# Kernel tuning notes

Measured on AMD Instinct MI355X. Metric: run time of the kernel, lower is better.

Reference implementation:

```python
import jax, jax.numpy as jnp
import numpy as np

N_FR, N_FV, N_REL, N_VAL, N_KN = 512, 512, 256, 256, 512
TOPK_FR, TOPK_FV, TOPK_REL, TOPK_VAL = 8, 8, 4, 6
EPS = 1e-8


def setup_inputs() -> dict:
    key = jax.random.key(0)
    k1, k2, k3, k4 = jax.random.split(key, 4)
    B, S, D, DS = 8, 2048, 2048, 64
    N = N_FR + N_FV + N_REL + N_VAL + N_KN  # 2304
    return {
        "x": jax.random.normal(k1, (B, S, D), dtype=jnp.float32),
        "importance": jax.random.uniform(k2, (B, S), dtype=jnp.float32),
        "W": jax.random.normal(k3, (DS, D), dtype=jnp.float32) * (1.0 / np.sqrt(D)),
        "b": jnp.zeros((DS,), dtype=jnp.float32),
        "neuron_emb": jax.random.normal(k4, (N, DS), dtype=jnp.float32) * 0.02,
    }


def _topk_sparsify(w, k):
    # w: [B, n] -> keep top-k values, zero the rest, renormalize to sum 1
    vals, idx = jax.lax.top_k(w, k)
    B = w.shape[0]
    sparse = jnp.zeros_like(w).at[jnp.arange(B)[:, None], idx].set(vals)
    return sparse / (sparse.sum(axis=-1, keepdims=True) + EPS)


def reference(x, importance, W, b, neuron_emb):
    # Projection (nn.Linear): [B,S,d_space]; dropout is identity in eval mode
    h = jnp.einsum('bsd,kd->bsk', x, W) + b
    # Normalized neuron embeddings (F.normalize along dim=-1)
    emb = neuron_emb / jnp.linalg.norm(neuron_emb, axis=-1, keepdims=True)
    # All routing logits in one shot: [B, S, total_neurons]
    all_logits = jnp.einsum('bsk,nk->bsn', h, emb)

    fr_end = N_FR
    fv_end = N_FR + N_FV
    rel_end = fv_end + N_REL
    val_end = rel_end + N_VAL

    fr_pref = jax.nn.softmax(all_logits[..., :fr_end], axis=-1)
    fv_pref = jax.nn.softmax(all_logits[..., fr_end:fv_end], axis=-1)
    rel_pref = jax.nn.softmax(all_logits[..., fv_end:rel_end], axis=-1)  # shared by Q and K
    val_pref = jax.nn.softmax(all_logits[..., rel_end:val_end], axis=-1)

    def dense(pref):
        return jnp.einsum('bs,bsn->bn', importance, pref)

    fr_w = _topk_sparsify(dense(fr_pref), TOPK_FR)
    fv_w = _topk_sparsify(dense(fv_pref), TOPK_FV)
    rel_d = dense(rel_pref)
    rq_w = _topk_sparsify(rel_d, TOPK_REL)
    rk_w = rq_w  # relational_Q and relational_K slices are identical
    val_w = _topk_sparsify(dense(val_pref), TOPK_VAL)

    # Concatenate the five per-batch routing weight vectors: [B, 512+512+256+256+256]
    return jnp.concatenate([fr_w, fv_w, rq_w, rk_w, val_w], axis=-1)
```

## Files before the change

### kernel.cpp

```cpp
#include <hip/hip_runtime.h>
#include <hip/hip_bf16.h>

#define B_    8
#define S_    2048
#define D_    2048
#define DS_   64
#define NUSED 1536
#define TOK   16384

typedef __attribute__((ext_vector_type(8))) short bf16x8;
typedef __attribute__((ext_vector_type(4))) float f32x4;

static constexpr int WS_ETF  = 0;
static constexpr int WS_HT   = 98304;
static constexpr int WS_PART = 2195456;
static constexpr int WS_PART2= 3768320;
static constexpr int WS_WF   = 3866624;

typedef __attribute__((address_space(1))) const void g_void;
typedef __attribute__((address_space(3))) void l_void;

__device__ inline short bf_hi(float f, float& rhi) {
    __hip_bfloat16 h = __float2bfloat16(f);
    rhi = __bfloat162float(h);
    return __builtin_bit_cast(short, h);
}
__device__ inline short bf_of(float f) {
    __hip_bfloat16 h = __float2bfloat16(f);
    return __builtin_bit_cast(short, h);
}
__device__ inline int sliceOfTile(int tile) {
    return tile < 32 ? 0 : tile < 64 ? 1 : tile < 80 ? 2 : 3;
}

__launch_bounds__(256)
__global__ void k_pre(const float* __restrict__ emb, const float* __restrict__ W,
                      short* __restrict__ etfrag, short* __restrict__ wfrag) {
    __shared__ float red[2][16][8];
    __shared__ float rn[2][16];
    const int tid = threadIdx.x;
    if (blockIdx.x < 48) {
        const int tl = tid >> 7, tid2 = tid & 127;
        const int kh = tid2 >> 6, lane = tid2 & 63;
        const int tile = blockIdx.x * 2 + tl;
        const int nl = lane & 15;
        const int n = tile * 16 + nl;
        const int kb = kh * 32 + (lane >> 4) * 8;
        const float* ep = emb + n * DS_ + kb;
        float4 a = *reinterpret_cast<const float4*>(ep);
        float4 b = *reinterpret_cast<const float4*>(ep + 4);
        float f[8] = {a.x, a.y, a.z, a.w, b.x, b.y, b.z, b.w};
        float ss = 0.f;
#pragma unroll
        for (int j = 0; j < 8; ++j) ss += f[j] * f[j];
        red[tl][nl][kh * 4 + (lane >> 4)] = ss;
        __syncthreads();
        if (tid2 < 16) {
            float s = 0.f;
#pragma unroll
            for (int j = 0; j < 8; ++j) s += red[tl][tid2][j];
            rn[tl][tid2] = 1.0f / sqrtf(s);
        }
        __syncthreads();
        const float r0 = rn[tl][nl];
        bf16x8 hi, lo;
#pragma unroll
        for (int j = 0; j < 8; ++j) {
            float v = f[j] * r0, r;
            hi[j] = bf_hi(v, r);
            lo[j] = bf_of(v - r);
        }
        short* dst = etfrag + (size_t)((tile * 2 + kh) * 64 + lane) * 16;
        *reinterpret_cast<bf16x8*>(dst)     = hi;
        *reinterpret_cast<bf16x8*>(dst + 8) = lo;
    } else {
        const int kstep = blockIdx.x - 48;
        const int msub = tid >> 6, lane = tid & 63;
        const int m = msub * 16 + (lane & 15);
        const float* wp = W + m * D_ + kstep * 32 + (lane >> 4) * 8;
        float4 a = *reinterpret_cast<const float4*>(wp);
        float4 b = *reinterpret_cast<const float4*>(wp + 4);
        float f[8] = {a.x, a.y, a.z, a.w, b.x, b.y, b.z, b.w};
        bf16x8 hi, lo;
#pragma unroll
        for (int j = 0; j < 8; ++j) {
            float r;
            hi[j] = bf_hi(f[j], r);
            lo[j] = bf_of(f[j] - r);
        }
        short* base = wfrag + (size_t)(kstep * 4 + msub) * 1024;
        *reinterpret_cast<bf16x8*>(base + lane * 8)       = hi;
        *reinterpret_cast<bf16x8*>(base + 512 + lane * 8) = lo;
    }
}

#define MFMA16(A, Bv, C) __builtin_amdgcn_mfma_f32_16x16x32_bf16(A, Bv, C, 0, 0, 0)

__launch_bounds__(256, 2)
__global__ void k_gemm1(const float* __restrict__ x, const short* __restrict__ wfrag,
                        float* __restrict__ htp) {
    __shared__ short wlds[2][2][4096];

    const int tid   = threadIdx.x;
    const int split = blockIdx.x & 1;
    const int tb    = (blockIdx.x >> 1) * 64;
    const int wave  = tid >> 6, lane = tid & 63;
    const int tok   = tb + wave * 16 + (lane & 15);

    const float* xp   = x + (size_t)tok * D_ + split * 1024 + (lane >> 4) * 8;
    const short* wsrc = wfrag + (size_t)(split * 32) * 4096;

    f32x4 acc0 = {0.f, 0.f, 0.f, 0.f};
    f32x4 acc1 = acc0, acc2 = acc0, acc3 = acc0;

#define STAGE(g, buf)                                                                        \
    {                                                                                        \
        const short* s0 = wsrc + (size_t)(2 * (g)) * 4096;                                   \
        __builtin_amdgcn_global_load_lds((g_void*)(s0 + tid * 8),                            \
                                         (l_void*)(&wlds[buf][0][tid * 8]), 16, 0, 0);       \
        __builtin_amdgcn_global_load_lds((g_void*)(s0 + 2048 + tid * 8),                     \
                                         (l_void*)(&wlds[buf][0][2048 + tid * 8]), 16, 0, 0);\
        __builtin_amdgcn_global_load_lds((g_void*)(s0 + 4096 + tid * 8),                     \
                                         (l_void*)(&wlds[buf][1][tid * 8]), 16, 0, 0);       \
        __builtin_amdgcn_global_load_lds((g_void*)(s0 + 6144 + tid * 8),                     \
                                         (l_void*)(&wlds[buf][1][2048 + tid * 8]), 16, 0, 0);\
    }

    STAGE(0, 0);
    float4 xc0 = *reinterpret_cast<const float4*>(xp);
    float4 xc1 = *reinterpret_cast<const float4*>(xp + 4);
    float4 xc2 = *reinterpret_cast<const float4*>(xp + 32);
    float4 xc3 = *reinterpret_cast<const float4*>(xp + 36);

#pragma unroll 2
    for (int g = 0; g < 16; ++g) {
        __syncthreads();
        const int buf = g & 1;
        float4 xn0, xn1, xn2, xn3;
        if (g < 15) {
            STAGE(g + 1, buf ^ 1);
            const float* nxp = xp + (size_t)(g + 1) * 64;
            xn0 = *reinterpret_cast<const float4*>(nxp);
            xn1 = *reinterpret_cast<const float4*>(nxp + 4);
            xn2 = *reinterpret_cast<const float4*>(nxp + 32);
            xn3 = *reinterpret_cast<const float4*>(nxp + 36);
        }
#pragma unroll
        for (int kk = 0; kk < 2; ++kk) {
            const float4 va = kk ? xc2 : xc0;
            const float4 vb = kk ? xc3 : xc1;
            float xf[8] = {va.x, va.y, va.z, va.w, vb.x, vb.y, vb.z, vb.w};
            bf16x8 bh, bl;
#pragma unroll
            for (int j = 0; j < 8; ++j) {
                float r;
                bh[j] = bf_hi(xf[j], r);
                bl[j] = bf_of(xf[j] - r);
            }
            const short* wl = &wlds[buf][kk][0];
            bf16x8 ah0 = *reinterpret_cast<const bf16x8*>(wl +    0 + lane * 8);
            bf16x8 al0 = *reinterpret_cast<const bf16x8*>(wl +  512 + lane * 8);
            bf16x8 ah1 = *reinterpret_cast<const bf16x8*>(wl + 1024 + lane * 8);
            bf16x8 al1 = *reinterpret_cast<const bf16x8*>(wl + 1536 + lane * 8);
            bf16x8 ah2 = *reinterpret_cast<const bf16x8*>(wl + 2048 + lane * 8);
            bf16x8 al2 = *reinterpret_cast<const bf16x8*>(wl + 2560 + lane * 8);
            bf16x8 ah3 = *reinterpret_cast<const bf16x8*>(wl + 3072 + lane * 8);
            bf16x8 al3 = *reinterpret_cast<const bf16x8*>(wl + 3584 + lane * 8);

            acc0 = MFMA16(ah0, bh, acc0);
            acc1 = MFMA16(ah1, bh, acc1);
            acc2 = MFMA16(ah2, bh, acc2);
            acc3 = MFMA16(ah3, bh, acc3);
            acc0 = MFMA16(al0, bh, acc0);
            acc1 = MFMA16(al1, bh, acc1);
            acc2 = MFMA16(al2, bh, acc2);
            acc3 = MFMA16(al3, bh, acc3);
            acc0 = MFMA16(ah0, bl, acc0);
            acc1 = MFMA16(ah1, bl, acc1);
            acc2 = MFMA16(ah2, bl, acc2);
            acc3 = MFMA16(ah3, bl, acc3);
        }
        if (g < 15) { xc0 = xn0; xc1 = xn1; xc2 = xn2; xc3 = xn3; }
    }

    const int row0 = split * 64 + (lane >> 4) * 4;
    const int col  = tb + wave * 16 + (lane & 15);
#pragma unroll
    for (int r = 0; r < 4; ++r) {
        htp[(size_t)(row0 +  0 + r) * TOK + col] = acc0[r];
        htp[(size_t)(row0 + 16 + r) * TOK + col] = acc1[r];
        htp[(size_t)(row0 + 32 + r) * TOK + col] = acc2[r];
        htp[(size_t)(row0 + 48 + r) * TOK + col] = acc3[r];
    }
}

__launch_bounds__(512, 2)
__global__ void k_route2(const float* __restrict__ htp, const float* __restrict__ bias,
                         const short* __restrict__ etfrag, const float* __restrict__ imp,
                         float* __restrict__ part) {
    __shared__ float h_lds[64][16];
    __shared__ float zw[8][2][16];
    __shared__ float coef[4][16];
    __shared__ float impb[16];

    const int tid = threadIdx.x;
    const int w = tid >> 6, lane = tid & 63;
    const int tt = blockIdx.x;
    const int tk = lane & 15, g = lane >> 4;

    if (tid < 256) {
        const int k = tid >> 2, t4 = (tid & 3) << 2;
        const float4* hp4 = reinterpret_cast<const float4*>(htp);
        const int col = tt * 4 + (tid & 3);
        float4 a = hp4[(size_t)k * 4096 + col];
        float4 b = hp4[(size_t)(k + 64) * 4096 + col];
        float bk = bias[k];
        float4 s;
        s.x = a.x + b.x + bk;
        s.y = a.y + b.y + bk;
        s.z = a.z + b.z + bk;
        s.w = a.w + b.w + bk;
        *reinterpret_cast<float4*>(&h_lds[k][t4]) = s;
    }
    if (tid < 16) impb[tid] = imp[tt * 16 + tid];
    __syncthreads();

    bf16x8 bh0, bl0, bh1, bl1;
#pragma unroll
    for (int j = 0; j < 8; ++j) {
        float r;
        float v0 = h_lds[g * 8 + j][tk];
        bh0[j] = bf_hi(v0, r);
        bl0[j] = bf_of(v0 - r);
        float v1 = h_lds[32 + g * 8 + j][tk];
        bh1[j] = bf_hi(v1, r);
        bl1[j] = bf_of(v1 - r);
    }

    const int t0 = w * 12;
    const int sA = sliceOfTile(t0);
    const int sB = sliceOfTile(t0 + 11);
    float zacc0 = 0.f, zacc1 = 0.f;
    float p[12][4];

    const short* ep = etfrag + (size_t)t0 * 2048 + lane * 16;
#pragma unroll
    for (int ti = 0; ti < 12; ++ti) {
        const short* cp = ep + (size_t)ti * 2048;
        bf16x8 ah0 = *reinterpret_cast<const bf16x8*>(cp);
        bf16x8 al0 = *reinterpret_cast<const bf16x8*>(cp + 8);
        bf16x8 ah1 = *reinterpret_cast<const bf16x8*>(cp + 1024);
        bf16x8 al1 = *reinterpret_cast<const bf16x8*>(cp + 1032);
        f32x4 a0 = {0.f, 0.f, 0.f, 0.f};
        f32x4 a1 = {0.f, 0.f, 0.f, 0.f};
        a0 = MFMA16(ah0, bh0, a0);
        a1 = MFMA16(ah1, bh1, a1);
        a0 = MFMA16(al0, bh0, a0);
        a1 = MFMA16(al1, bh1, a1);
        a0 = MFMA16(ah0, bl0, a0);
        a1 = MFMA16(ah1, bl1, a1);
        const float p0 = __expf(a0[0] + a1[0]);
        const float p1 = __expf(a0[1] + a1[1]);
        const float p2 = __expf(a0[2] + a1[2]);
        const float p3 = __expf(a0[3] + a1[3]);
        p[ti][0] = p0; p[ti][1] = p1; p[ti][2] = p2; p[ti][3] = p3;
        const float zs = (p0 + p1) + (p2 + p3);
        if (sliceOfTile(t0 + ti) == sA) zacc0 += zs; else zacc1 += zs;
    }

    zacc0 += __shfl_xor(zacc0, 16); zacc0 += __shfl_xor(zacc0, 32);
    zacc1 += __shfl_xor(zacc1, 16); zacc1 += __shfl_xor(zacc1, 32);
    if (lane < 16) { zw[w][0][lane] = zacc0; zw[w][1][lane] = zacc1; }
    __syncthreads();

    if (tid < 64) {
        const int s = tid >> 4, k2 = tid & 15;
        float z = 0.f;
#pragma unroll
        for (int w2 = 0; w2 < 8; ++w2) {
            const int a = sliceOfTile(w2 * 12);
            const int b = sliceOfTile(w2 * 12 + 11);
            if (a == s) z += zw[w2][0][k2];
            if (b == s && b != a) z += zw[w2][1][k2];
        }
        coef[s][k2] = impb[k2] / z;
    }
    __syncthreads();

    const float cA = coef[sA][tk];
    const float cB = coef[sB][tk];
    float* pout = part + (size_t)tt * NUSED;
#pragma unroll
    for (int ti = 0; ti < 12; ++ti) {
        const float c = (sliceOfTile(t0 + ti) == sA) ? cA : cB;
        float v0 = p[ti][0] * c, v1 = p[ti][1] * c, v2 = p[ti][2] * c, v3 = p[ti][3] * c;
#pragma unroll
        for (int st = 1; st < 16; st <<= 1) {
            v0 += __shfl_xor(v0, st);
            v1 += __shfl_xor(v1, st);
            v2 += __shfl_xor(v2, st);
            v3 += __shfl_xor(v3, st);
        }
        if (tk == 0)
            *reinterpret_cast<float4*>(&pout[(t0 + ti) * 16 + g * 4]) =
                make_float4(v0, v1, v2, v3);
    }
}

__launch_bounds__(256)
__global__ void kA(const float* __restrict__ part, float* __restrict__ part2) {
    const int tid = threadIdx.x;
    const int b = blockIdx.x >> 3, g = blockIdx.x & 7;
    const int base = (b * 128 + g * 16) * NUSED;
#pragma unroll
    for (int i = 0; i < 6; ++i) {
        int n = tid + 256 * i;
        float s = 0.f;
#pragma unroll
        for (int r = 0; r < 16; ++r) s += part[base + r * NUSED + n];
        part2[(b * 8 + g) * NUSED + n] = s;
    }
}

__launch_bounds__(256)
__global__ void kB(const float* __restrict__ part2, float* __restrict__ out) {
    __shared__ float dens[NUSED];
    __shared__ float s_v[4][8];
    __shared__ int   s_n[4][8];
    const int tid = threadIdx.x;
    const int b = blockIdx.x;

#pragma unroll
    for (int i = 0; i < 6; ++i) {
        int n = tid + 256 * i;
        float s = 0.f;
#pragma unroll
        for (int g = 0; g < 8; ++g) s += part2[(b * 8 + g) * NUSED + n];
        dens[n] = s;
    }
    for (int i = tid; i < 1792; i += 256) out[b * 1792 + i] = 0.f;
    __syncthreads();

    const int w = tid >> 6, lane = tid & 63;
    const int soffs[4] = {0, 512, 1024, 1280};
    const int ssz[4]   = {512, 512, 256, 256};
    const int kks[4]   = {8, 8, 4, 6};
    const int ooffs[4] = {0, 512, 1024, 1536};
    const int Sn = ssz[w], soff = soffs[w], kk = kks[w];
    const int nslots = Sn >> 6;

    float v[8];
#pragma unroll
    for (int i = 0; i < 8; ++i)
        v[i] = (i < nslots) ? dens[soff + lane + 64 * i] : -1e30f;

    unsigned rm = 0;
    float ssum = 0.f;
    for (int it = 0; it < kk; ++it) {
        float bv = -1e30f;
        int bn = 0x7fffffff;
#pragma unroll
        for (int i = 0; i < 8; ++i) {
            bool valid = (i < nslots) && !((rm >> i) & 1u);
            if (valid && v[i] > bv) { bv = v[i]; bn = lane + 64 * i; }
        }
#pragma unroll
        for (int off = 32; off; off >>= 1) {
            float ov = __shfl_xor(bv, off);
            int   on = __shfl_xor(bn, off);
            if (ov > bv || (ov == bv && on < bn)) { bv = ov; bn = on; }
        }
        ssum += bv;
        if ((bn & 63) == lane) rm |= 1u << (bn >> 6);
        if (lane == 0) { s_v[w][it] = bv; s_n[w][it] = bn; }
    }
    const float inv = 1.f / (ssum + 1e-8f);
    if (lane < kk) {
        int n = s_n[w][lane];
        float val = s_v[w][lane] * inv;
        out[b * 1792 + ooffs[w] + n] = val;
        if (w == 2) out[b * 1792 + 1280 + n] = val;
    }
}

extern "C" void kernel_launch(void* const* d_in, const int* in_sizes, int n_in,
                              void* d_out, int out_size, void* d_ws, size_t ws_size,
                              hipStream_t stream) {
    const float* x    = (const float*)d_in[0];
    const float* imp  = (const float*)d_in[1];
    const float* W    = (const float*)d_in[2];
    const float* bias = (const float*)d_in[3];
    const float* emb  = (const float*)d_in[4];
    float* out = (float*)d_out;
    float* ws  = (float*)d_ws;

    short* etfrag = (short*)(ws + WS_ETF);
    float* htp    = ws + WS_HT;
    float* part   = ws + WS_PART;
    float* part2  = ws + WS_PART2;
    short* wfrag  = (short*)(ws + WS_WF);

    k_pre<<<112, 256, 0, stream>>>(emb, W, etfrag, wfrag);
    k_gemm1<<<512, 256, 0, stream>>>(x, wfrag, htp);
    k_route2<<<1024, 512, 0, stream>>>(htp, bias, etfrag, imp, part);
    kA<<<64, 256, 0, stream>>>(part, part2);
    kB<<<8, 256, 0, stream>>>(part2, out);
}
```

Measured before the change: 77.42 us.

## Fuse projection GEMM into routing kernel, keeping h in LDS

Merges the x·W projection kernel into the routing kernel. Each 512-thread block computes h for its 16 tokens directly: 8 waves split into 4 output subtiles times 2 K-halves, and the partial sums are reduced in LDS together with the bias. This removes the global round-trip of the 64x16384 h intermediate and one kernel launch. In exchange, W fragments are re-read from global/L2 by every block without LDS staging or double buffering, and each wave now does a long serial K loop with a single accumulator chain.

```diff
diff --git a/kernel.cpp b/kernel.cpp
--- a/kernel.cpp
+++ b/kernel.cpp
@@ -11,11 +11,10 @@
 typedef __attribute__((ext_vector_type(8))) short bf16x8;
 typedef __attribute__((ext_vector_type(4))) float f32x4;
 
-static constexpr int WS_ETF  = 0;
-static constexpr int WS_HT   = 98304;
-static constexpr int WS_PART = 2195456;
-static constexpr int WS_PART2= 3768320;
-static constexpr int WS_WF   = 3866624;
+static constexpr int WS_ETF   = 0;
+static constexpr int WS_WF    = 98304;
+static constexpr int WS_PART  = 229376;
+static constexpr int WS_PART2 = 1802240;
 
 typedef __attribute__((address_space(1))) const void g_void;
 typedef __attribute__((address_space(3))) void l_void;
@@ -96,60 +95,38 @@
 
 #define MFMA16(A, Bv, C) __builtin_amdgcn_mfma_f32_16x16x32_bf16(A, Bv, C, 0, 0, 0)
 
-__launch_bounds__(256, 2)
-__global__ void k_gemm1(const float* __restrict__ x, const short* __restrict__ wfrag,
-                        float* __restrict__ htp) {
-    __shared__ short wlds[2][2][4096];
-
-    const int tid   = threadIdx.x;
-    const int split = blockIdx.x & 1;
-    const int tb    = (blockIdx.x >> 1) * 64;
-    const int wave  = tid >> 6, lane = tid & 63;
-    const int tok   = tb + wave * 16 + (lane & 15);
-
-    const float* xp   = x + (size_t)tok * D_ + split * 1024 + (lane >> 4) * 8;
-    const short* wsrc = wfrag + (size_t)(split * 32) * 4096;
-
-    f32x4 acc0 = {0.f, 0.f, 0.f, 0.f};
-    f32x4 acc1 = acc0, acc2 = acc0, acc3 = acc0;
-
-#define STAGE(g, buf)                                                                        \
-    {                                                                                        \
-        const short* s0 = wsrc + (size_t)(2 * (g)) * 4096;                                   \
-        __builtin_amdgcn_global_load_lds((g_void*)(s0 + tid * 8),                            \
-                                         (l_void*)(&wlds[buf][0][tid * 8]), 16, 0, 0);       \
-        __builtin_amdgcn_global_load_lds((g_void*)(s0 + 2048 + tid * 8),                     \
-                                         (l_void*)(&wlds[buf][0][2048 + tid * 8]), 16, 0, 0);\
-        __builtin_amdgcn_global_load_lds((g_void*)(s0 + 4096 + tid * 8),                     \
-                                         (l_void*)(&wlds[buf][1][tid * 8]), 16, 0, 0);       \
-        __builtin_amdgcn_global_load_lds((g_void*)(s0 + 6144 + tid * 8),                     \
-                                         (l_void*)(&wlds[buf][1][2048 + tid * 8]), 16, 0, 0);\
-    }
-
-    STAGE(0, 0);
-    float4 xc0 = *reinterpret_cast<const float4*>(xp);
-    float4 xc1 = *reinterpret_cast<const float4*>(xp + 4);
-    float4 xc2 = *reinterpret_cast<const float4*>(xp + 32);
-    float4 xc3 = *reinterpret_cast<const float4*>(xp + 36);
-
-#pragma unroll 2
-    for (int g = 0; g < 16; ++g) {
-        __syncthreads();
-        const int buf = g & 1;
-        float4 xn0, xn1, xn2, xn3;
-        if (g < 15) {
-            STAGE(g + 1, buf ^ 1);
-            const float* nxp = xp + (size_t)(g + 1) * 64;
-            xn0 = *reinterpret_cast<const float4*>(nxp);
-            xn1 = *reinterpret_cast<const float4*>(nxp + 4);
-            xn2 = *reinterpret_cast<const float4*>(nxp + 32);
-            xn3 = *reinterpret_cast<const float4*>(nxp + 36);
-        }
-#pragma unroll
-        for (int kk = 0; kk < 2; ++kk) {
-            const float4 va = kk ? xc2 : xc0;
-            const float4 vb = kk ? xc3 : xc1;
-            float xf[8] = {va.x, va.y, va.z, va.w, vb.x, vb.y, vb.z, vb.w};
+__launch_bounds__(512, 4)
+__global__ void k_fused(const float* __restrict__ x, const short* __restrict__ wfrag,
+                        const float* __restrict__ bias, const short* __restrict__ etfrag,
+                        const float* __restrict__ imp, float* __restrict__ part) {
+    __shared__ float hpart[2][64][16];
+    __shared__ float biasl[64];
+    __shared__ float zw[8][2][16];
+    __shared__ float coef[4][16];
+    __shared__ float impb[16];
+
+    const int tid = threadIdx.x;
+    const int w = tid >> 6, lane = tid & 63;
+    const int tt = blockIdx.x;
+    const int tk = lane & 15, g = lane >> 4;
+
+    if (tid < 64) biasl[tid] = bias[tid];
+    if (tid < 16) impb[tid] = imp[tt * 16 + tid];
+
+    {
+        const int msub = w & 3, khalf = w >> 2;
+        const int tok = tt * 16 + tk;
+        const float* xp = x + (size_t)tok * D_ + khalf * 1024 + g * 8;
+        const short* wp = wfrag + (size_t)(khalf * 32 * 4 + msub) * 1024 + lane * 8;
+        f32x4 acc = {0.f, 0.f, 0.f, 0.f};
+#pragma unroll 4
+        for (int ks = 0; ks < 32; ++ks) {
+            const short* wk = wp + (size_t)ks * 4096;
+            bf16x8 ah = *reinterpret_cast<const bf16x8*>(wk);
+            bf16x8 al = *reinterpret_cast<const bf16x8*>(wk + 512);
+            float4 xa = *reinterpret_cast<const float4*>(xp + ks * 32);
+            float4 xb = *reinterpret_cast<const float4*>(xp + ks * 32 + 4);
+            float xf[8] = {xa.x, xa.y, xa.z, xa.w, xb.x, xb.y, xb.z, xb.w};
             bf16x8 bh, bl;
 #pragma unroll
             for (int j = 0; j < 8; ++j) {
@@ -157,82 +134,24 @@
                 bh[j] = bf_hi(xf[j], r);
                 bl[j] = bf_of(xf[j] - r);
             }
-            const short* wl = &wlds[buf][kk][0];
-            bf16x8 ah0 = *reinterpret_cast<const bf16x8*>(wl +    0 + lane * 8);
-            bf16x8 al0 = *reinterpret_cast<const bf16x8*>(wl +  512 + lane * 8);
-            bf16x8 ah1 = *reinterpret_cast<const bf16x8*>(wl + 1024 + lane * 8);
-            bf16x8 al1 = *reinterpret_cast<const bf16x8*>(wl + 1536 + lane * 8);
-            bf16x8 ah2 = *reinterpret_cast<const bf16x8*>(wl + 2048 + lane * 8);
-            bf16x8 al2 = *reinterpret_cast<const bf16x8*>(wl + 2560 + lane * 8);
-            bf16x8 ah3 = *reinterpret_cast<const bf16x8*>(wl + 3072 + lane * 8);
-            bf16x8 al3 = *reinterpret_cast<const bf16x8*>(wl + 3584 + lane * 8);
-
-            acc0 = MFMA16(ah0, bh, acc0);
-            acc1 = MFMA16(ah1, bh, acc1);
-            acc2 = MFMA16(ah2, bh, acc2);
-            acc3 = MFMA16(ah3, bh, acc3);
-            acc0 = MFMA16(al0, bh, acc0);
-            acc1 = MFMA16(al1, bh, acc1);
-            acc2 = MFMA16(al2, bh, acc2);
-            acc3 = MFMA16(al3, bh, acc3);
-            acc0 = MFMA16(ah0, bl, acc0);
-            acc1 = MFMA16(ah1, bl, acc1);
-            acc2 = MFMA16(ah2, bl, acc2);
-            acc3 = MFMA16(ah3, bl, acc3);
-        }
-        if (g < 15) { xc0 = xn0; xc1 = xn1; xc2 = xn2; xc3 = xn3; }
-    }
-
-    const int row0 = split * 64 + (lane >> 4) * 4;
-    const int col  = tb + wave * 16 + (lane & 15);
-#pragma unroll
-    for (int r = 0; r < 4; ++r) {
-        htp[(size_t)(row0 +  0 + r) * TOK + col] = acc0[r];
-        htp[(size_t)(row0 + 16 + r) * TOK + col] = acc1[r];
-        htp[(size_t)(row0 + 32 + r) * TOK + col] = acc2[r];
-        htp[(size_t)(row0 + 48 + r) * TOK + col] = acc3[r];
-    }
-}
-
-__launch_bounds__(512, 2)
-__global__ void k_route2(const float* __restrict__ htp, const float* __restrict__ bias,
-                         const short* __restrict__ etfrag, const float* __restrict__ imp,
-                         float* __restrict__ part) {
-    __shared__ float h_lds[64][16];
-    __shared__ float zw[8][2][16];
-    __shared__ float coef[4][16];
-    __shared__ float impb[16];
-
-    const int tid = threadIdx.x;
-    const int w = tid >> 6, lane = tid & 63;
-    const int tt = blockIdx.x;
-    const int tk = lane & 15, g = lane >> 4;
-
-    if (tid < 256) {
-        const int k = tid >> 2, t4 = (tid & 3) << 2;
-        const float4* hp4 = reinterpret_cast<const float4*>(htp);
-        const int col = tt * 4 + (tid & 3);
-        float4 a = hp4[(size_t)k * 4096 + col];
-        float4 b = hp4[(size_t)(k + 64) * 4096 + col];
-        float bk = bias[k];
-        float4 s;
-        s.x = a.x + b.x + bk;
-        s.y = a.y + b.y + bk;
-        s.z = a.z + b.z + bk;
-        s.w = a.w + b.w + bk;
-        *reinterpret_cast<float4*>(&h_lds[k][t4]) = s;
-    }
-    if (tid < 16) impb[tid] = imp[tt * 16 + tid];
+            acc = MFMA16(ah, bh, acc);
+            acc = MFMA16(al, bh, acc);
+            acc = MFMA16(ah, bl, acc);
+        }
+#pragma unroll
+        for (int r = 0; r < 4; ++r)
+            hpart[khalf][msub * 16 + g * 4 + r][tk] = acc[r];
+    }
     __syncthreads();
 
     bf16x8 bh0, bl0, bh1, bl1;
 #pragma unroll
     for (int j = 0; j < 8; ++j) {
         float r;
-        float v0 = h_lds[g * 8 + j][tk];
+        float v0 = hpart[0][g * 8 + j][tk] + hpart[1][g * 8 + j][tk] + biasl[g * 8 + j];
         bh0[j] = bf_hi(v0, r);
         bl0[j] = bf_of(v0 - r);
-        float v1 = h_lds[32 + g * 8 + j][tk];
+        float v1 = hpart[0][32 + g * 8 + j][tk] + hpart[1][32 + g * 8 + j][tk] + biasl[32 + g * 8 + j];
         bh1[j] = bf_hi(v1, r);
         bl1[j] = bf_of(v1 - r);
     }
@@ -395,14 +314,12 @@
     float* ws  = (float*)d_ws;
 
     short* etfrag = (short*)(ws + WS_ETF);
-    float* htp    = ws + WS_HT;
+    short* wfrag  = (short*)(ws + WS_WF);
     float* part   = ws + WS_PART;
     float* part2  = ws + WS_PART2;
-    short* wfrag  = (short*)(ws + WS_WF);
 
     k_pre<<<112, 256, 0, stream>>>(emb, W, etfrag, wfrag);
-    k_gemm1<<<512, 256, 0, stream>>>(x, wfrag, htp);
-    k_route2<<<1024, 512, 0, stream>>>(htp, bias, etfrag, imp, part);
+    k_fused<<<1024, 512, 0, stream>>>(x, wfrag, bias, etfrag, imp, part);
     kA<<<64, 256, 0, stream>>>(part, part2);
     kB<<<8, 256, 0, stream>>>(part2, out);
 }
```

New measurement: 115.8 us. 1.5x slower.

## Double routing tokens per block and stage four W k-steps per barrier

Applied to the files above, without the earlier changes.

k_route2 now handles 32 tokens per block instead of 16. Each embedding fragment loaded from global memory is reused for two token tiles, and the grid is halved. k_gemm1 stages four k-slices of W fragments per LDS buffer, so it runs 8 synchronised iterations instead of 16. This cuts barrier count and embedding reloads, but raises register pressure in k_route2 (two sets of 12x4 probabilities) and doubles the LDS footprint in k_gemm1, which may lower occupancy.

```diff
diff --git a/kernel.cpp b/kernel.cpp
--- a/kernel.cpp
+++ b/kernel.cpp
@@ -99,7 +99,7 @@
 __launch_bounds__(256, 2)
 __global__ void k_gemm1(const float* __restrict__ x, const short* __restrict__ wfrag,
                         float* __restrict__ htp) {
-    __shared__ short wlds[2][2][4096];
+    __shared__ short wlds[2][4][4096];
 
     const int tid   = threadIdx.x;
     const int split = blockIdx.x & 1;
@@ -113,74 +113,78 @@
     f32x4 acc0 = {0.f, 0.f, 0.f, 0.f};
     f32x4 acc1 = acc0, acc2 = acc0, acc3 = acc0;
 
-#define STAGE(g, buf)                                                                        \
+#define STAGE4(gg, buf)                                                                      \
     {                                                                                        \
-        const short* s0 = wsrc + (size_t)(2 * (g)) * 4096;                                   \
-        __builtin_amdgcn_global_load_lds((g_void*)(s0 + tid * 8),                            \
-                                         (l_void*)(&wlds[buf][0][tid * 8]), 16, 0, 0);       \
-        __builtin_amdgcn_global_load_lds((g_void*)(s0 + 2048 + tid * 8),                     \
-                                         (l_void*)(&wlds[buf][0][2048 + tid * 8]), 16, 0, 0);\
-        __builtin_amdgcn_global_load_lds((g_void*)(s0 + 4096 + tid * 8),                     \
-                                         (l_void*)(&wlds[buf][1][tid * 8]), 16, 0, 0);       \
-        __builtin_amdgcn_global_load_lds((g_void*)(s0 + 6144 + tid * 8),                     \
-                                         (l_void*)(&wlds[buf][1][2048 + tid * 8]), 16, 0, 0);\
-    }
-
-    STAGE(0, 0);
-    float4 xc0 = *reinterpret_cast<const float4*>(xp);
-    float4 xc1 = *reinterpret_cast<const float4*>(xp + 4);
-    float4 xc2 = *reinterpret_cast<const float4*>(xp + 32);
-    float4 xc3 = *reinterpret_cast<const float4*>(xp + 36);
-
-#pragma unroll 2
-    for (int g = 0; g < 16; ++g) {
+        _Pragma("unroll")                                                                    \
+        for (int s = 0; s < 4; ++s) {                                                        \
+            const short* s0 = wsrc + (size_t)(4 * (gg) + s) * 4096;                          \
+            __builtin_amdgcn_global_load_lds((g_void*)(s0 + tid * 8),                        \
+                                             (l_void*)(&wlds[buf][s][tid * 8]), 16, 0, 0);   \
+            __builtin_amdgcn_global_load_lds((g_void*)(s0 + 2048 + tid * 8),                 \
+                                             (l_void*)(&wlds[buf][s][2048 + tid * 8]), 16, 0, 0); \
+        }                                                                                    \
+    }
+
+    STAGE4(0, 0);
+    float4 xc[4], xn[4];
+#pragma unroll
+    for (int i = 0; i < 4; ++i)
+        xc[i] = *reinterpret_cast<const float4*>(xp + (i >> 1) * 32 + (i & 1) * 4);
+
+    for (int g = 0; g < 8; ++g) {
         __syncthreads();
         const int buf = g & 1;
-        float4 xn0, xn1, xn2, xn3;
-        if (g < 15) {
-            STAGE(g + 1, buf ^ 1);
-            const float* nxp = xp + (size_t)(g + 1) * 64;
-            xn0 = *reinterpret_cast<const float4*>(nxp);
-            xn1 = *reinterpret_cast<const float4*>(nxp + 4);
-            xn2 = *reinterpret_cast<const float4*>(nxp + 32);
-            xn3 = *reinterpret_cast<const float4*>(nxp + 36);
-        }
-#pragma unroll
-        for (int kk = 0; kk < 2; ++kk) {
-            const float4 va = kk ? xc2 : xc0;
-            const float4 vb = kk ? xc3 : xc1;
-            float xf[8] = {va.x, va.y, va.z, va.w, vb.x, vb.y, vb.z, vb.w};
-            bf16x8 bh, bl;
-#pragma unroll
-            for (int j = 0; j < 8; ++j) {
-                float r;
-                bh[j] = bf_hi(xf[j], r);
-                bl[j] = bf_of(xf[j] - r);
+        if (g < 7) STAGE4(g + 1, buf ^ 1);
+
+#pragma unroll
+        for (int half = 0; half < 2; ++half) {
+            const int hh = g * 2 + half;
+            if (hh < 15) {
+                const float* nxp = xp + (size_t)(hh + 1) * 64;
+#pragma unroll
+                for (int i = 0; i < 4; ++i)
+                    xn[i] = *reinterpret_cast<const float4*>(nxp + (i >> 1) * 32 + (i & 1) * 4);
             }
-            const short* wl = &wlds[buf][kk][0];
-            bf16x8 ah0 = *reinterpret_cast<const bf16x8*>(wl +    0 + lane * 8);
-            bf16x8 al0 = *reinterpret_cast<const bf16x8*>(wl +  512 + lane * 8);
-            bf16x8 ah1 = *reinterpret_cast<const bf16x8*>(wl + 1024 + lane * 8);
-            bf16x8 al1 = *reinterpret_cast<const bf16x8*>(wl + 1536 + lane * 8);
-            bf16x8 ah2 = *reinterpret_cast<const bf16x8*>(wl + 2048 + lane * 8);
-            bf16x8 al2 = *reinterpret_cast<const bf16x8*>(wl + 2560 + lane * 8);
-            bf16x8 ah3 = *reinterpret_cast<const bf16x8*>(wl + 3072 + lane * 8);
-            bf16x8 al3 = *reinterpret_cast<const bf16x8*>(wl + 3584 + lane * 8);
-
-            acc0 = MFMA16(ah0, bh, acc0);
-            acc1 = MFMA16(ah1, bh, acc1);
-            acc2 = MFMA16(ah2, bh, acc2);
-            acc3 = MFMA16(ah3, bh, acc3);
-            acc0 = MFMA16(al0, bh, acc0);
-            acc1 = MFMA16(al1, bh, acc1);
-            acc2 = MFMA16(al2, bh, acc2);
-            acc3 = MFMA16(al3, bh, acc3);
-            acc0 = MFMA16(ah0, bl, acc0);
-            acc1 = MFMA16(ah1, bl, acc1);
-            acc2 = MFMA16(ah2, bl, acc2);
-            acc3 = MFMA16(ah3, bl, acc3);
-        }
-        if (g < 15) { xc0 = xn0; xc1 = xn1; xc2 = xn2; xc3 = xn3; }
+#pragma unroll
+            for (int kk2 = 0; kk2 < 2; ++kk2) {
+                const int kk = half * 2 + kk2;
+                const float4 va = xc[kk2 * 2], vb = xc[kk2 * 2 + 1];
+                float xf[8] = {va.x, va.y, va.z, va.w, vb.x, vb.y, vb.z, vb.w};
+                bf16x8 bh, bl;
+#pragma unroll
+                for (int j = 0; j < 8; ++j) {
+                    float r;
+                    bh[j] = bf_hi(xf[j], r);
+                    bl[j] = bf_of(xf[j] - r);
+                }
+                const short* wl = &wlds[buf][kk][0];
+                bf16x8 ah0 = *reinterpret_cast<const bf16x8*>(wl +    0 + lane * 8);
+                bf16x8 al0 = *reinterpret_cast<const bf16x8*>(wl +  512 + lane * 8);
+                bf16x8 ah1 = *reinterpret_cast<const bf16x8*>(wl + 1024 + lane * 8);
+                bf16x8 al1 = *reinterpret_cast<const bf16x8*>(wl + 1536 + lane * 8);
+                bf16x8 ah2 = *reinterpret_cast<const bf16x8*>(wl + 2048 + lane * 8);
+                bf16x8 al2 = *reinterpret_cast<const bf16x8*>(wl + 2560 + lane * 8);
+                bf16x8 ah3 = *reinterpret_cast<const bf16x8*>(wl + 3072 + lane * 8);
+                bf16x8 al3 = *reinterpret_cast<const bf16x8*>(wl + 3584 + lane * 8);
+
+                acc0 = MFMA16(ah0, bh, acc0);
+                acc1 = MFMA16(ah1, bh, acc1);
+                acc2 = MFMA16(ah2, bh, acc2);
+                acc3 = MFMA16(ah3, bh, acc3);
+                acc0 = MFMA16(al0, bh, acc0);
+                acc1 = MFMA16(al1, bh, acc1);
+                acc2 = MFMA16(al2, bh, acc2);
+                acc3 = MFMA16(al3, bh, acc3);
+                acc0 = MFMA16(ah0, bl, acc0);
+                acc1 = MFMA16(ah1, bl, acc1);
+                acc2 = MFMA16(ah2, bl, acc2);
+                acc3 = MFMA16(ah3, bl, acc3);
+            }
+            if (hh < 15) {
+#pragma unroll
+                for (int i = 0; i < 4; ++i) xc[i] = xn[i];
+            }
+        }
     }
 
     const int row0 = split * 64 + (lane >> 4) * 4;
@@ -194,24 +198,24 @@
     }
 }
 
-__launch_bounds__(512, 2)
+__launch_bounds__(512)
 __global__ void k_route2(const float* __restrict__ htp, const float* __restrict__ bias,
                          const short* __restrict__ etfrag, const float* __restrict__ imp,
                          float* __restrict__ part) {
-    __shared__ float h_lds[64][16];
-    __shared__ float zw[8][2][16];
-    __shared__ float coef[4][16];
-    __shared__ float impb[16];
+    __shared__ float h_lds[64][32];
+    __shared__ float zw[2][8][2][16];
+    __shared__ float coef[2][4][16];
+    __shared__ float impb[32];
 
     const int tid = threadIdx.x;
     const int w = tid >> 6, lane = tid & 63;
-    const int tt = blockIdx.x;
+    const int tt2 = blockIdx.x;
     const int tk = lane & 15, g = lane >> 4;
 
-    if (tid < 256) {
-        const int k = tid >> 2, t4 = (tid & 3) << 2;
+    {
+        const int k = tid >> 3, c8 = tid & 7;
         const float4* hp4 = reinterpret_cast<const float4*>(htp);
-        const int col = tt * 4 + (tid & 3);
+        const int col = tt2 * 8 + c8;
         float4 a = hp4[(size_t)k * 4096 + col];
         float4 b = hp4[(size_t)(k + 64) * 4096 + col];
         float bk = bias[k];
@@ -220,28 +224,26 @@
         s.y = a.y + b.y + bk;
         s.z = a.z + b.z + bk;
         s.w = a.w + b.w + bk;
-        *reinterpret_cast<float4*>(&h_lds[k][t4]) = s;
-    }
-    if (tid < 16) impb[tid] = imp[tt * 16 + tid];
+        *reinterpret_cast<float4*>(&h_lds[k][c8 * 4]) = s;
+    }
+    if (tid < 32) impb[tid] = imp[tt2 * 32 + tid];
     __syncthreads();
 
-    bf16x8 bh0, bl0, bh1, bl1;
+    bf16x8 bh0A, bl0A, bh1A, bl1A, bh0B, bl0B, bh1B, bl1B;
 #pragma unroll
     for (int j = 0; j < 8; ++j) {
-        float r;
-        float v0 = h_lds[g * 8 + j][tk];
-        bh0[j] = bf_hi(v0, r);
-        bl0[j] = bf_of(v0 - r);
-        float v1 = h_lds[32 + g * 8 + j][tk];
-        bh1[j] = bf_hi(v1, r);
-        bl1[j] = bf_of(v1 - r);
+        float r, v;
+        v = h_lds[g * 8 + j][tk];           bh0A[j] = bf_hi(v, r); bl0A[j] = bf_of(v - r);
+        v = h_lds[32 + g * 8 + j][tk];      bh1A[j] = bf_hi(v, r); bl1A[j] = bf_of(v - r);
+        v = h_lds[g * 8 + j][16 + tk];      bh0B[j] = bf_hi(v, r); bl0B[j] = bf_of(v - r);
+        v = h_lds[32 + g * 8 + j][16 + tk]; bh1B[j] = bf_hi(v, r); bl1B[j] = bf_of(v - r);
     }
 
     const int t0 = w * 12;
     const int sA = sliceOfTile(t0);
     const int sB = sliceOfTile(t0 + 11);
-    float zacc0 = 0.f, zacc1 = 0.f;
-    float p[12][4];
+    float zA0 = 0.f, zA1 = 0.f, zB0 = 0.f, zB1 = 0.f;
+    float pA[12][4], pB[12][4];
 
     const short* ep = etfrag + (size_t)t0 * 2048 + lane * 16;
 #pragma unroll
@@ -252,58 +254,89 @@
         bf16x8 ah1 = *reinterpret_cast<const bf16x8*>(cp + 1024);
         bf16x8 al1 = *reinterpret_cast<const bf16x8*>(cp + 1032);
         f32x4 a0 = {0.f, 0.f, 0.f, 0.f};
-        f32x4 a1 = {0.f, 0.f, 0.f, 0.f};
-        a0 = MFMA16(ah0, bh0, a0);
-        a1 = MFMA16(ah1, bh1, a1);
-        a0 = MFMA16(al0, bh0, a0);
-        a1 = MFMA16(al1, bh1, a1);
-        a0 = MFMA16(ah0, bl0, a0);
-        a1 = MFMA16(ah1, bl1, a1);
-        const float p0 = __expf(a0[0] + a1[0]);
-        const float p1 = __expf(a0[1] + a1[1]);
-        const float p2 = __expf(a0[2] + a1[2]);
-        const float p3 = __expf(a0[3] + a1[3]);
-        p[ti][0] = p0; p[ti][1] = p1; p[ti][2] = p2; p[ti][3] = p3;
-        const float zs = (p0 + p1) + (p2 + p3);
-        if (sliceOfTile(t0 + ti) == sA) zacc0 += zs; else zacc1 += zs;
-    }
-
-    zacc0 += __shfl_xor(zacc0, 16); zacc0 += __shfl_xor(zacc0, 32);
-    zacc1 += __shfl_xor(zacc1, 16); zacc1 += __shfl_xor(zacc1, 32);
-    if (lane < 16) { zw[w][0][lane] = zacc0; zw[w][1][lane] = zacc1; }
+        f32x4 a1 = a0, b0 = a0, b1 = a0;
+        a0 = MFMA16(ah0, bh0A, a0);  b0 = MFMA16(ah0, bh0B, b0);
+        a1 = MFMA16(ah1, bh1A, a1);  b1 = MFMA16(ah1, bh1B, b1);
+        a0 = MFMA16(al0, bh0A, a0);  b0 = MFMA16(al0, bh0B, b0);
+        a1 = MFMA16(al1, bh1A, a1);  b1 = MFMA16(al1, bh1B, b1);
+        a0 = MFMA16(ah0, bl0A, a0);  b0 = MFMA16(ah0, bl0B, b0);
+        a1 = MFMA16(ah1, bl1A, a1);  b1 = MFMA16(ah1, bl1B, b1);
+
+        const float pa0 = __expf(a0[0] + a1[0]);
+        const float pa1 = __expf(a0[1] + a1[1]);
+        const float pa2 = __expf(a0[2] + a1[2]);
+        const float pa3 = __expf(a0[3] + a1[3]);
+        pA[ti][0] = pa0; pA[ti][1] = pa1; pA[ti][2] = pa2; pA[ti][3] = pa3;
+        const float zsA = (pa0 + pa1) + (pa2 + pa3);
+        const float pb0 = __expf(b0[0] + b1[0]);
+        const float pb1 = __expf(b0[1] + b1[1]);
+        const float pb2 = __expf(b0[2] + b1[2]);
+        const float pb3 = __expf(b0[3] + b1[3]);
+        pB[ti][0] = pb0; pB[ti][1] = pb1; pB[ti][2] = pb2; pB[ti][3] = pb3;
+        const float zsB = (pb0 + pb1) + (pb2 + pb3);
+        if (sliceOfTile(t0 + ti) == sA) { zA0 += zsA; zB0 += zsB; }
+        else                            { zA1 += zsA; zB1 += zsB; }
+    }
+
+    zA0 += __shfl_xor(zA0, 16); zA0 += __shfl_xor(zA0, 32);
+    zA1 += __shfl_xor(zA1, 16); zA1 += __shfl_xor(zA1, 32);
+    zB0 += __shfl_xor(zB0, 16); zB0 += __shfl_xor(zB0, 32);
+    zB1 += __shfl_xor(zB1, 16); zB1 += __shfl_xor(zB1, 32);
+    if (lane < 16) {
+        zw[0][w][0][lane] = zA0; zw[0][w][1][lane] = zA1;
+        zw[1][w][0][lane] = zB0; zw[1][w][1][lane] = zB1;
+    }
     __syncthreads();
 
-    if (tid < 64) {
-        const int s = tid >> 4, k2 = tid & 15;
+    if (tid < 128) {
+        const int tl = tid >> 6, s = (tid >> 4) & 3, k2 = tid & 15;
         float z = 0.f;
 #pragma unroll
         for (int w2 = 0; w2 < 8; ++w2) {
             const int a = sliceOfTile(w2 * 12);
             const int b = sliceOfTile(w2 * 12 + 11);
-            if (a == s) z += zw[w2][0][k2];
-            if (b == s && b != a) z += zw[w2][1][k2];
-        }
-        coef[s][k2] = impb[k2] / z;
+            if (a == s) z += zw[tl][w2][0][k2];
+            if (b == s && b != a) z += zw[tl][w2][1][k2];
+        }
+        coef[tl][s][k2] = impb[tl * 16 + k2] / z;
     }
     __syncthreads();
 
-    const float cA = coef[sA][tk];
-    const float cB = coef[sB][tk];
-    float* pout = part + (size_t)tt * NUSED;
+    const float cAA = coef[0][sA][tk], cAB = coef[0][sB][tk];
+    const float cBA = coef[1][sA][tk], cBB = coef[1][sB][tk];
+    float* poutA = part + (size_t)(tt2 * 2) * NUSED;
+    float* poutB = poutA + NUSED;
 #pragma unroll
     for (int ti = 0; ti < 12; ++ti) {
-        const float c = (sliceOfTile(t0 + ti) == sA) ? cA : cB;
-        float v0 = p[ti][0] * c, v1 = p[ti][1] * c, v2 = p[ti][2] * c, v3 = p[ti][3] * c;
-#pragma unroll
-        for (int st = 1; st < 16; st <<= 1) {
-            v0 += __shfl_xor(v0, st);
-            v1 += __shfl_xor(v1, st);
-            v2 += __shfl_xor(v2, st);
-            v3 += __shfl_xor(v3, st);
-        }
-        if (tk == 0)
-            *reinterpret_cast<float4*>(&pout[(t0 + ti) * 16 + g * 4]) =
-                make_float4(v0, v1, v2, v3);
+        const bool inA = (sliceOfTile(t0 + ti) == sA);
+        {
+            const float c = inA ? cAA : cAB;
+            float v0 = pA[ti][0] * c, v1 = pA[ti][1] * c, v2 = pA[ti][2] * c, v3 = pA[ti][3] * c;
+#pragma unroll
+            for (int st = 1; st < 16; st <<= 1) {
+                v0 += __shfl_xor(v0, st);
+                v1 += __shfl_xor(v1, st);
+                v2 += __shfl_xor(v2, st);
+                v3 += __shfl_xor(v3, st);
+            }
+            if (tk == 0)
+                *reinterpret_cast<float4*>(&poutA[(t0 + ti) * 16 + g * 4]) =
+                    make_float4(v0, v1, v2, v3);
+        }
+        {
+            const float c = inA ? cBA : cBB;
+            float v0 = pB[ti][0] * c, v1 = pB[ti][1] * c, v2 = pB[ti][2] * c, v3 = pB[ti][3] * c;
+#pragma unroll
+            for (int st = 1; st < 16; st <<= 1) {
+                v0 += __shfl_xor(v0, st);
+                v1 += __shfl_xor(v1, st);
+                v2 += __shfl_xor(v2, st);
+                v3 += __shfl_xor(v3, st);
+            }
+            if (tk == 0)
+                *reinterpret_cast<float4*>(&poutB[(t0 + ti) * 16 + g * 4]) =
+                    make_float4(v0, v1, v2, v3);
+        }
     }
 }
 
@@ -402,7 +435,7 @@
 
     k_pre<<<112, 256, 0, stream>>>(emb, W, etfrag, wfrag);
     k_gemm1<<<512, 256, 0, stream>>>(x, wfrag, htp);
-    k_route2<<<1024, 512, 0, stream>>>(htp, bias, etfrag, imp, part);
+    k_route2<<<512, 512, 0, stream>>>(htp, bias, etfrag, imp, part);
     kA<<<64, 256, 0, stream>>>(part, part2);
     kB<<<8, 256, 0, stream>>>(part2, out);
 }
```

Result: slower. 79.37 us (+2.5%).
